# Kernel optimization log

Hardware: AMD Instinct MI355X
Metric: run time of the kernel (lower is better)

Reference implementation:

```python
import jax, jax.numpy as jnp
import numpy as np

N_NODES = 50000
N_EDGES = 1600000
IN_CH = 128
HEADS = 4
OUT_PER_HEAD = 32  # out_channels // heads with concat=True
NEG_SLOPE = 0.2    # GATConv default leaky_relu slope
SOFTMAX_EPS = 1e-16  # PyG scatter-softmax denominator eps
LN_EPS = 1e-5


def setup_inputs() -> dict:
    key = jax.random.key(0)
    ks = jax.random.split(key, 8)
    x = jax.random.normal(ks[0], (N_NODES, IN_CH), dtype=jnp.float32)
    edge_index = jax.random.randint(ks[1], (2, N_EDGES), 0, N_NODES, dtype=jnp.int32)
    W = jax.random.normal(ks[2], (IN_CH, HEADS * OUT_PER_HEAD), dtype=jnp.float32) * (1.0 / np.sqrt(IN_CH))
    att_src = jax.random.normal(ks[3], (HEADS, OUT_PER_HEAD), dtype=jnp.float32) * 0.1
    att_dst = jax.random.normal(ks[4], (HEADS, OUT_PER_HEAD), dtype=jnp.float32) * 0.1
    bias = jnp.zeros((HEADS * OUT_PER_HEAD,), dtype=jnp.float32)
    gamma = jnp.ones((HEADS * OUT_PER_HEAD,), dtype=jnp.float32)
    beta = jnp.zeros((HEADS * OUT_PER_HEAD,), dtype=jnp.float32)
    return {"x": x, "edge_index": edge_index, "W": W, "att_src": att_src,
            "att_dst": att_dst, "bias": bias, "gamma": gamma, "beta": beta}


def reference(x, edge_index, W, att_src, att_dst, bias, gamma, beta):
    N = x.shape[0]
    H, C = att_src.shape
    # GATConv default add_self_loops=True
    loop = jnp.arange(N, dtype=edge_index.dtype)
    src = jnp.concatenate([edge_index[0], loop])  # message source j
    dst = jnp.concatenate([edge_index[1], loop])  # aggregation target i

    h = (x @ W).reshape(N, H, C)                      # [N,H,C]
    a_s = jnp.einsum('nhc,hc->nh', h, att_src)        # [N,H]
    a_d = jnp.einsum('nhc,hc->nh', h, att_dst)        # [N,H]

    logits = jax.nn.leaky_relu(a_s[src] + a_d[dst], NEG_SLOPE)  # [E,H]
    # segment softmax over edges grouped by destination node
    m = jax.ops.segment_max(logits, dst, num_segments=N)        # [N,H]
    m = jnp.where(jnp.isfinite(m), m, 0.0)
    e = jnp.exp(logits - m[dst])
    s = jax.ops.segment_sum(e, dst, num_segments=N)             # [N,H]
    alpha = e / (s[dst] + SOFTMAX_EPS)                          # [E,H]

    msg = h[src] * alpha[:, :, None]                            # [E,H,C]
    out = jax.ops.segment_sum(msg, dst, num_segments=N)         # [N,H,C]
    out = out.reshape(N, H * C) + bias

    mu = out.mean(axis=-1, keepdims=True)
    var = ((out - mu) ** 2).mean(axis=-1, keepdims=True)
    y = (out - mu) / jnp.sqrt(var + LN_EPS) * gamma + beta
    return jax.nn.elu(y)
```

## Files before the change

kernel.cpp:

```cpp
#include <hip/hip_runtime.h>
#include <hip/hip_bf16.h>

typedef __hip_bfloat16 bf16;
typedef unsigned int u32;
typedef unsigned short u16;
typedef __attribute__((ext_vector_type(8))) short bf16x8;
typedef __attribute__((ext_vector_type(4))) float f32x4;

constexpr int N   = 50000;
constexpr int E   = 1600000;
constexpr int C   = 128;
constexpr int H   = 4;
constexpr int NB  = 782;
constexpr int CAP = 2560;
constexpr int NCH = 256;
constexpr int CHUNK = E / NCH;
constexpr int WT_COLS = 144;
constexpr float NEG  = 0.2f;
constexpr float SEPS = 1e-16f;
constexpr float LEPS = 1e-5f;

__device__ __forceinline__ float lo16(u32 v) { return __uint_as_float(v << 16); }
__device__ __forceinline__ float hi16(u32 v) { return __uint_as_float(v & 0xFFFF0000u); }
__device__ __forceinline__ u16 bfbits(float f) {
    __hip_bfloat16 h = __float2bfloat16(f);
    return *reinterpret_cast<u16*>(&h);
}

__global__ __launch_bounds__(256) void k0_wprep(
    const float* __restrict__ W,
    const float* __restrict__ att_s, const float* __restrict__ att_d,
    u16* __restrict__ wt_hi, u16* __restrict__ wt_lo)
{
    const int i = blockIdx.x * 256 + threadIdx.x;
    if (i >= WT_COLS * 128) return;
    const int c = i >> 7, k = i & 127;
    float w = 0.f;
    if (c < 128) {
        w = W[k * 128 + c];
    } else if (c < 136) {
        const int vc = c - 128;
        const int h = vc & 3;
        const float* att = (vc < 4) ? att_s : att_d;
        float s = 0.f;
#pragma unroll
        for (int j = 0; j < 32; ++j)
            s = fmaf(W[k * 128 + h * 32 + j], att[h * 32 + j], s);
        w = s;
    }
    const __hip_bfloat16 h = __float2bfloat16(w);
    const float fh = __bfloat162float(h);
    wt_hi[i] = *(const u16*)&h;
    wt_lo[i] = bfbits(w - fh);
}

__global__ __launch_bounds__(256, 2) void kg_gemm(
    const float* __restrict__ x,
    const u16* __restrict__ wt_hi, const u16* __restrict__ wt_lo,
    u16* __restrict__ hb, float* __restrict__ as_, float* __restrict__ ad_)
{
    const int t    = threadIdx.x;
    const int m0   = (int)blockIdx.x * 64;
    const int lane = t & 63;
    const int w    = t >> 6;
    const int bcol = lane & 15;
    const int akg  = lane >> 4;
    const int aq   = akg;

    const int arow = min(m0 + w * 16 + bcol, N - 1);
    const float* xr = x + (size_t)arow * 128;

    float4 q[8];
#pragma unroll
    for (int ks = 0; ks < 4; ++ks) {
        q[2 * ks]     = *(const float4*)(xr + ks * 32 + akg * 8);
        q[2 * ks + 1] = *(const float4*)(xr + ks * 32 + akg * 8 + 4);
    }
    __builtin_amdgcn_sched_barrier(0);

    f32x4 acc[9];
#pragma unroll
    for (int nt = 0; nt < 9; ++nt) acc[nt] = f32x4{0.f, 0.f, 0.f, 0.f};

#pragma unroll
    for (int ks = 0; ks < 4; ++ks) {
        const float4 q0 = q[2 * ks];
        const float4 q1 = q[2 * ks + 1];
        bf16x8 Ah, Al;
#define CV(idx, val) { const __hip_bfloat16 hh = __float2bfloat16(val); \
        Ah[idx] = *(const short*)&hh; \
        const __hip_bfloat16 hl = __float2bfloat16((val) - __bfloat162float(hh)); \
        Al[idx] = *(const short*)&hl; }
        CV(0, q0.x) CV(1, q0.y) CV(2, q0.z) CV(3, q0.w)
        CV(4, q1.x) CV(5, q1.y) CV(6, q1.z) CV(7, q1.w)
#undef CV
        const u16* bpk = wt_hi + bcol * 128 + ks * 32 + akg * 8;
        const u16* bqk = wt_lo + bcol * 128 + ks * 32 + akg * 8;
#pragma unroll
        for (int nt = 0; nt < 9; ++nt) {
            const bf16x8 Bh = *(const bf16x8*)(bpk + nt * 2048);
            const bf16x8 Bl = *(const bf16x8*)(bqk + nt * 2048);
            acc[nt] = __builtin_amdgcn_mfma_f32_16x16x32_bf16(Ah, Bh, acc[nt], 0, 0, 0);
            acc[nt] = __builtin_amdgcn_mfma_f32_16x16x32_bf16(Al, Bh, acc[nt], 0, 0, 0);
            acc[nt] = __builtin_amdgcn_mfma_f32_16x16x32_bf16(Ah, Bl, acc[nt], 0, 0, 0);
        }
    }

#pragma unroll
    for (int nt = 0; nt < 8; ++nt) {
        const int ch = nt * 16 + bcol;
#pragma unroll
        for (int r = 0; r < 4; ++r) {
            const int node = m0 + w * 16 + aq * 4 + r;
            if (node < N) hb[(size_t)node * 128 + ch] = bfbits(acc[nt][r]);
        }
    }

    if (bcol < 8) {
        float* dst = (bcol < 4) ? (as_ + bcol) : (ad_ + (bcol - 4));
#pragma unroll
        for (int r = 0; r < 4; ++r) {
            const int node = m0 + w * 16 + aq * 4 + r;
            if (node < N) dst[(size_t)node * H] = acc[8][r];
        }
    }
}

__global__ __launch_bounds__(256) void kc_count(
    const int* __restrict__ ei, u32* __restrict__ gcnt)
{
    __shared__ u32 lcnt[NB];
    const int t = threadIdx.x;
    const int c = blockIdx.x;
    const int base = c * CHUNK;
    for (int i = t; i < NB; i += 256) lcnt[i] = 0;
    __syncthreads();
    for (int i = t; i < CHUNK; i += 256)
        atomicAdd(&lcnt[((u32)ei[E + base + i]) >> 6], 1u);
    __syncthreads();
    for (int i = t; i < NB; i += 256) gcnt[i * NCH + c] = lcnt[i];
}

__global__ __launch_bounds__(256) void s2a_scan(
    const u32* __restrict__ gcnt, u32* __restrict__ gbase, u32* __restrict__ tot)
{
    __shared__ u32 wsum[4];
    const int b = blockIdx.x, t = threadIdx.x, lane = t & 63, w = t >> 6;
    const u32 v = gcnt[b * NCH + t];
    u32 incl = v;
#pragma unroll
    for (int off = 1; off < 64; off <<= 1) {
        u32 u = __shfl_up(incl, off, 64);
        if (lane >= off) incl += u;
    }
    if (lane == 63) wsum[w] = incl;
    __syncthreads();
    u32 wpre = 0;
#pragma unroll
    for (int i = 0; i < 4; ++i) if (i < w) wpre += wsum[i];
    gbase[b * NCH + t] = wpre + incl - v;
    if (t == 255) tot[b] = wpre + incl;
}

__global__ __launch_bounds__(64) void s2b_scan(
    const u32* __restrict__ tot, u32* __restrict__ bbase)
{
    const int t = threadIdx.x;
    u32 vals[13];
    u32 s = 0;
#pragma unroll
    for (int i = 0; i < 13; ++i) {
        int idx = t * 13 + i;
        u32 v = (idx < NB) ? tot[idx] : 0u;
        vals[i] = s; s += v;
    }
    u32 incl = s;
#pragma unroll
    for (int off = 1; off < 64; off <<= 1) {
        u32 u = __shfl_up(incl, off, 64);
        if (t >= off) incl += u;
    }
    const u32 excl = incl - s;
#pragma unroll
    for (int i = 0; i < 13; ++i) {
        int idx = t * 13 + i;
        if (idx < NB) bbase[idx] = excl + vals[i];
    }
}

__global__ __launch_bounds__(256) void kbinB(
    const int* __restrict__ ei, const u32* __restrict__ gbase,
    const u32* __restrict__ bbase, u32* __restrict__ pairs)
{
    __shared__ u32 sl[NB];
    __shared__ u32 lfill[NB];
    const int t = threadIdx.x;
    const int c = blockIdx.x;

    for (int i = t; i < NB; i += 256) {
        sl[i] = bbase[i] + gbase[(size_t)i * NCH + c];
        lfill[i] = 0u;
    }
    __syncthreads();

    const int base = c * CHUNK;
    for (int i = t; i < CHUNK; i += 256) {
        const u32 src = (u32)ei[base + i];
        const u32 dst = (u32)ei[E + base + i];
        const u32 b = dst >> 6;
        const u32 pos = atomicAdd(&lfill[b], 1u);
        pairs[sl[b] + pos] = src | ((dst & 63u) << 16);
    }
}

__global__ __launch_bounds__(256) void kfill2(
    const u32* __restrict__ pairs, const u32* __restrict__ tot,
    const u32* __restrict__ bbase, int* __restrict__ row_ptr, u16* __restrict__ col)
{
    __shared__ u32 spr[CAP];
    __shared__ u16 scol[CAP];
    __shared__ int jcnt[64], joff[64], jcur[64];
    const int b = blockIdx.x, t = threadIdx.x;
    const int base = (int)bbase[b];
    const int cntb = (int)tot[b];
    if (t < 64) jcnt[t] = 0;
    __syncthreads();

    const u32* pr = pairs + base;
    for (int i = t; i < cntb; i += 256) spr[i] = pr[i];
    __syncthreads();
    for (int i = t; i < cntb; i += 256) atomicAdd(&jcnt[spr[i] >> 16], 1);
    __syncthreads();
    if (t < 64) {
        int v = jcnt[t], incl = v;
#pragma unroll
        for (int off = 1; off < 64; off <<= 1) {
            int u = __shfl_up(incl, off, 64);
            if (t >= off) incl += u;
        }
        joff[t] = incl - v;
        const int n = b * 64 + t;
        if (n < N) row_ptr[n] = base + joff[t];
        jcur[t] = 0;
    }
    __syncthreads();
    for (int i = t; i < cntb; i += 256) {
        const u32 p = spr[i];
        const int j = p >> 16;
        const int pos = atomicAdd(&jcur[j], 1);
        scol[joff[j] + pos] = (u16)(p & 0xFFFFu);
    }
    __syncthreads();
    for (int i = t; i < cntb; i += 256) col[base + i] = scol[i];
    if (b == 0 && t == 0) row_ptr[N] = E;
}

__global__ __launch_bounds__(256) void kd_agg_ln(
    const int* __restrict__ row_ptr, const u16* __restrict__ col,
    const u32* __restrict__ hb, const float* __restrict__ as_,
    const float* __restrict__ ad_,
    const float* __restrict__ bias, const float* __restrict__ gamma,
    const float* __restrict__ beta, float* __restrict__ out, int n0)
{
    __shared__ float wlds[4][64];
    const int tid  = threadIdx.x;
    const int lane = tid & 63;
    const int wv   = __builtin_amdgcn_readfirstlane(tid >> 6);
    const int n    = __builtin_amdgcn_readfirstlane(n0 + (int)blockIdx.x * 4 + (tid >> 6));
    if (n >= N) return;

    const int head  = lane >> 4;
    const int eoff  = lane & 15;
    const int wbase = head << 4;
    float* __restrict__ wrow = wlds[wv];

    const float adn = ad_[n * H + head];
    const float asn = as_[n * H + head];

    float ls = asn + adn;
    ls = fmaxf(ls, NEG * ls);
    const float wself = __expf(ls);
    float den = (eoff == 0) ? wself : 0.f;
    const u32 hvs = hb[n * 64 + lane];
    float num0 = wself * lo16(hvs);
    float num1 = wself * hi16(hvs);

    const int k0  = row_ptr[n];
    const int deg = row_ptr[n + 1] - k0;
    const int ntiles = (deg + 15) >> 4;

    const int cnt0 = deg < 16 ? deg : 16;
    const int cnt1 = (deg - 16) < 16 ? (deg - 16) : 16;
    int colv_cur = (eoff < cnt0) ? (int)col[k0 + eoff]      : 0;
    int colv_nxt = (eoff < cnt1) ? (int)col[k0 + 16 + eoff] : 0;
    float a_cur  = as_[colv_cur * H + head];
    int cntc = cnt0, cntn = cnt1;

    int k = k0;
    for (int t = 0; t < ntiles; ++t, k += 16) {
        const int rem2 = deg - 16 * (t + 2);
        const int cnt2 = rem2 < 16 ? rem2 : 16;
        const int cf_raw = (int)col[k + 32 + eoff];
        const int colv_f = (eoff < cnt2) ? cf_raw : 0;

        float le = a_cur + adn;
        le = fmaxf(le, NEG * le);
        const float w = (eoff < cntc) ? __expf(le) : 0.f;
        den += w;
        wrow[lane] = w;
        const int colc = colv_cur;

#define GL(i) const u32* rp##i = hb + ((size_t)(u32)__builtin_amdgcn_readlane(colc, i) << 6); \
              const u32 v##i = rp##i[lane];
        GL(0) GL(1) GL(2) GL(3) GL(4) GL(5) GL(6) GL(7)
        GL(8) GL(9) GL(10) GL(11) GL(12) GL(13) GL(14) GL(15)
#undef GL
        __builtin_amdgcn_sched_barrier(0);

        const float a_n = as_[colv_nxt * H + head];
        __builtin_amdgcn_sched_barrier(0);

        {
            const float4 wa = *(const float4*)(wrow + wbase + 0);
            num0 = fmaf(wa.x, lo16(v0), num0);  num1 = fmaf(wa.x, hi16(v0), num1);
            num0 = fmaf(wa.y, lo16(v1), num0);  num1 = fmaf(wa.y, hi16(v1), num1);
            num0 = fmaf(wa.z, lo16(v2), num0);  num1 = fmaf(wa.z, hi16(v2), num1);
            num0 = fmaf(wa.w, lo16(v3), num0);  num1 = fmaf(wa.w, hi16(v3), num1);
            const float4 wb = *(const float4*)(wrow + wbase + 4);
            num0 = fmaf(wb.x, lo16(v4), num0);  num1 = fmaf(wb.x, hi16(v4), num1);
            num0 = fmaf(wb.y, lo16(v5), num0);  num1 = fmaf(wb.y, hi16(v5), num1);
            num0 = fmaf(wb.z, lo16(v6), num0);  num1 = fmaf(wb.z, hi16(v6), num1);
            num0 = fmaf(wb.w, lo16(v7), num0);  num1 = fmaf(wb.w, hi16(v7), num1);
            const float4 wc = *(const float4*)(wrow + wbase + 8);
            num0 = fmaf(wc.x, lo16(v8), num0);  num1 = fmaf(wc.x, hi16(v8), num1);
            num0 = fmaf(wc.y, lo16(v9), num0);  num1 = fmaf(wc.y, hi16(v9), num1);
            num0 = fmaf(wc.z, lo16(v10), num0); num1 = fmaf(wc.z, hi16(v10), num1);
            num0 = fmaf(wc.w, lo16(v11), num0); num1 = fmaf(wc.w, hi16(v11), num1);
            const float4 wd = *(const float4*)(wrow + wbase + 12);
            num0 = fmaf(wd.x, lo16(v12), num0); num1 = fmaf(wd.x, hi16(v12), num1);
            num0 = fmaf(wd.y, lo16(v13), num0); num1 = fmaf(wd.y, hi16(v13), num1);
            num0 = fmaf(wd.z, lo16(v14), num0); num1 = fmaf(wd.z, hi16(v14), num1);
            num0 = fmaf(wd.w, lo16(v15), num0); num1 = fmaf(wd.w, hi16(v15), num1);
        }

        colv_cur = colv_nxt; colv_nxt = colv_f;
        a_cur = a_n;
        cntc = cntn; cntn = cnt2;
    }

#pragma unroll
    for (int off = 1; off < 16; off <<= 1) den += __shfl_xor(den, off, 64);

    const int c0 = lane * 2;
    const float inv_den = 1.f / (den + SEPS);
    const float2 bi = *(const float2*)(bias + c0);
    float v0 = num0 * inv_den + bi.x;
    float v1 = num1 * inv_den + bi.y;

    float sum = v0 + v1;
#pragma unroll
    for (int off = 32; off; off >>= 1) sum += __shfl_xor(sum, off, 64);
    const float mu = sum * (1.0f / C);
    const float d0 = v0 - mu, d1 = v1 - mu;
    float sq = d0 * d0 + d1 * d1;
#pragma unroll
    for (int off = 32; off; off >>= 1) sq += __shfl_xor(sq, off, 64);
    const float inv = rsqrtf(sq * (1.0f / C) + LEPS);
    const float2 ga = *(const float2*)(gamma + c0);
    const float2 be = *(const float2*)(beta  + c0);
    float y0 = d0 * inv * ga.x + be.x;
    float y1 = d1 * inv * ga.y + be.y;
    y0 = y0 > 0.f ? y0 : __expf(y0) - 1.f;
    y1 = y1 > 0.f ? y1 : __expf(y1) - 1.f;
    float2 o; o.x = y0; o.y = y1;
    *(float2*)(out + (size_t)n * C + c0) = o;
}

extern "C" void kernel_launch(void* const* d_in, const int* in_sizes, int n_in,
                              void* d_out, int out_size, void* d_ws, size_t ws_size,
                              hipStream_t stream)
{
    const float* x     = (const float*)d_in[0];
    const int*   ei    = (const int*)  d_in[1];
    const float* W     = (const float*)d_in[2];
    const float* att_s = (const float*)d_in[3];
    const float* att_d = (const float*)d_in[4];
    const float* bias  = (const float*)d_in[5];
    const float* gamma = (const float*)d_in[6];
    const float* beta  = (const float*)d_in[7];
    float* out = (float*)d_out;

    char* p = (char*)d_ws;
    bf16*  hb      = (bf16*)p;   p += (size_t)N * C * sizeof(bf16);
    float* as_     = (float*)p;  p += (size_t)N * H * sizeof(float);
    float* ad_     = (float*)p;  p += (size_t)N * H * sizeof(float);
    u32*   pairs   = (u32*)p;    p += (size_t)E * sizeof(u32);
    u16*   col     = (u16*)p;    p += ((size_t)(E + 64) * sizeof(u16) + 15) & ~(size_t)15;
    int*   row_ptr = (int*)p;    p += ((size_t)(N + 1) * sizeof(int) + 15) & ~(size_t)15;
    u32*   gcnt    = (u32*)p;    p += (size_t)NB * NCH * sizeof(u32);
    u32*   gbase   = (u32*)p;    p += (size_t)NB * NCH * sizeof(u32);
    u32*   tot     = (u32*)p;    p += (((size_t)NB * sizeof(u32)) + 15) & ~(size_t)15;
    u32*   bbase   = (u32*)p;    p += (((size_t)NB * sizeof(u32)) + 15) & ~(size_t)15;
    u16*   wt_hi   = (u16*)p;    p += (size_t)WT_COLS * 128 * sizeof(u16);
    u16*   wt_lo   = (u16*)p;

    k0_wprep<<<(WT_COLS * 128 + 255) / 256, 256, 0, stream>>>(W, att_s, att_d, wt_hi, wt_lo);
    kg_gemm<<<NB, 256, 0, stream>>>(x, wt_hi, wt_lo, (u16*)hb, as_, ad_);
    kc_count<<<NCH, 256, 0, stream>>>(ei, gcnt);
    s2a_scan<<<NB, 256, 0, stream>>>(gcnt, gbase, tot);
    s2b_scan<<<1, 64, 0, stream>>>(tot, bbase);
    kbinB<<<NCH, 256, 0, stream>>>(ei, gbase, bbase, pairs);
    kfill2<<<NB, 256, 0, stream>>>(pairs, tot, bbase, row_ptr, col);
    kd_agg_ln<<<(25000 * 64) / 256, 256, 0, stream>>>(
        row_ptr, col, (const u32*)hb, as_, ad_, bias, gamma, beta, out, 0);
    kd_agg_ln<<<(25000 * 64) / 256, 256, 0, stream>>>(
        row_ptr, col, (const u32*)hb, as_, ad_, bias, gamma, beta, out, 25000);
}
```

Before: 227.8 us.

## Process two row tiles per wave in GEMM and double-buffer B fragments

The projection GEMM now handles 128 rows per block, with each wave computing two 16-row groups. This lets every B-fragment load from the split-bf16 weight tables be reused twice. B fragments for successive k-steps are prefetched into alternating register buffers, with schedule barriers to overlap loads with MFMA work. The cost is higher register pressure from 18 accumulators plus four B buffers, which may lower occupancy or cause spills. The grid also shrinks to about half as many blocks, which gives less parallelism for only 50k rows.

```diff
diff --git a/kernel.cpp b/kernel.cpp
--- a/kernel.cpp
+++ b/kernel.cpp
@@ -60,68 +60,108 @@
     u16* __restrict__ hb, float* __restrict__ as_, float* __restrict__ ad_)
 {
     const int t    = threadIdx.x;
-    const int m0   = (int)blockIdx.x * 64;
+    const int m0   = (int)blockIdx.x * 128;
     const int lane = t & 63;
     const int w    = t >> 6;
     const int bcol = lane & 15;
     const int akg  = lane >> 4;
-    const int aq   = akg;
-
-    const int arow = min(m0 + w * 16 + bcol, N - 1);
-    const float* xr = x + (size_t)arow * 128;
-
-    float4 q[8];
+
+    const int r0 = min(m0 + w * 32 + bcol,      N - 1);
+    const int r1 = min(m0 + w * 32 + 16 + bcol, N - 1);
+    const float* x0 = x + (size_t)r0 * 128 + akg * 8;
+    const float* x1 = x + (size_t)r1 * 128 + akg * 8;
+
+    float4 q[16];
 #pragma unroll
     for (int ks = 0; ks < 4; ++ks) {
-        q[2 * ks]     = *(const float4*)(xr + ks * 32 + akg * 8);
-        q[2 * ks + 1] = *(const float4*)(xr + ks * 32 + akg * 8 + 4);
+        q[4 * ks + 0] = *(const float4*)(x0 + ks * 32);
+        q[4 * ks + 1] = *(const float4*)(x0 + ks * 32 + 4);
+        q[4 * ks + 2] = *(const float4*)(x1 + ks * 32);
+        q[4 * ks + 3] = *(const float4*)(x1 + ks * 32 + 4);
     }
     __builtin_amdgcn_sched_barrier(0);
 
-    f32x4 acc[9];
-#pragma unroll
-    for (int nt = 0; nt < 9; ++nt) acc[nt] = f32x4{0.f, 0.f, 0.f, 0.f};
-
+    const u16* bp = wt_hi + bcol * 128 + akg * 8;
+    const u16* bq = wt_lo + bcol * 128 + akg * 8;
+    bf16x8 BhA[9], BlA[9], BhB[9], BlB[9];
+
+#define LOADB(BH, BL, ks)                                           \
+    _Pragma("unroll")                                               \
+    for (int nt = 0; nt < 9; ++nt) {                                \
+        BH[nt] = *(const bf16x8*)(bp + nt * 2048 + (ks) * 32);      \
+        BL[nt] = *(const bf16x8*)(bq + nt * 2048 + (ks) * 32);      \
+    }
+
+    LOADB(BhA, BlA, 0)
+    __builtin_amdgcn_sched_barrier(0);
+
+    bf16x8 Ah[2][4], Al[2][4];
 #pragma unroll
     for (int ks = 0; ks < 4; ++ks) {
-        const float4 q0 = q[2 * ks];
-        const float4 q1 = q[2 * ks + 1];
-        bf16x8 Ah, Al;
-#define CV(idx, val) { const __hip_bfloat16 hh = __float2bfloat16(val); \
-        Ah[idx] = *(const short*)&hh; \
-        const __hip_bfloat16 hl = __float2bfloat16((val) - __bfloat162float(hh)); \
-        Al[idx] = *(const short*)&hl; }
-        CV(0, q0.x) CV(1, q0.y) CV(2, q0.z) CV(3, q0.w)
-        CV(4, q1.x) CV(5, q1.y) CV(6, q1.z) CV(7, q1.w)
-#undef CV
-        const u16* bpk = wt_hi + bcol * 128 + ks * 32 + akg * 8;
-        const u16* bqk = wt_lo + bcol * 128 + ks * 32 + akg * 8;
-#pragma unroll
-        for (int nt = 0; nt < 9; ++nt) {
-            const bf16x8 Bh = *(const bf16x8*)(bpk + nt * 2048);
-            const bf16x8 Bl = *(const bf16x8*)(bqk + nt * 2048);
-            acc[nt] = __builtin_amdgcn_mfma_f32_16x16x32_bf16(Ah, Bh, acc[nt], 0, 0, 0);
-            acc[nt] = __builtin_amdgcn_mfma_f32_16x16x32_bf16(Al, Bh, acc[nt], 0, 0, 0);
-            acc[nt] = __builtin_amdgcn_mfma_f32_16x16x32_bf16(Ah, Bl, acc[nt], 0, 0, 0);
+#pragma unroll
+        for (int rg = 0; rg < 2; ++rg) {
+            const float4 qa = q[4 * ks + 2 * rg];
+            const float4 qb = q[4 * ks + 2 * rg + 1];
+            const float f[8] = {qa.x, qa.y, qa.z, qa.w, qb.x, qb.y, qb.z, qb.w};
+#pragma unroll
+            for (int j = 0; j < 8; ++j) {
+                const __hip_bfloat16 hh = __float2bfloat16(f[j]);
+                Ah[rg][ks][j] = *(const short*)&hh;
+                const __hip_bfloat16 hl = __float2bfloat16(f[j] - __bfloat162float(hh));
+                Al[rg][ks][j] = *(const short*)&hl;
+            }
         }
     }
 
-#pragma unroll
-    for (int nt = 0; nt < 8; ++nt) {
-        const int ch = nt * 16 + bcol;
-#pragma unroll
-        for (int r = 0; r < 4; ++r) {
-            const int node = m0 + w * 16 + aq * 4 + r;
-            if (node < N) hb[(size_t)node * 128 + ch] = bfbits(acc[nt][r]);
+    f32x4 acc[2][9];
+#pragma unroll
+    for (int rg = 0; rg < 2; ++rg)
+#pragma unroll
+        for (int nt = 0; nt < 9; ++nt) acc[rg][nt] = f32x4{0.f, 0.f, 0.f, 0.f};
+
+#define STEP(BHc, BLc, ks)                                          \
+    _Pragma("unroll")                                               \
+    for (int rg = 0; rg < 2; ++rg) {                                \
+        _Pragma("unroll")                                           \
+        for (int nt = 0; nt < 9; ++nt) {                            \
+            acc[rg][nt] = __builtin_amdgcn_mfma_f32_16x16x32_bf16(Ah[rg][ks], BHc[nt], acc[rg][nt], 0, 0, 0); \
+            acc[rg][nt] = __builtin_amdgcn_mfma_f32_16x16x32_bf16(Al[rg][ks], BHc[nt], acc[rg][nt], 0, 0, 0); \
+            acc[rg][nt] = __builtin_amdgcn_mfma_f32_16x16x32_bf16(Ah[rg][ks], BLc[nt], acc[rg][nt], 0, 0, 0); \
+        }                                                           \
+    }
+
+    LOADB(BhB, BlB, 1)
+    __builtin_amdgcn_sched_barrier(0);
+    STEP(BhA, BlA, 0)
+    LOADB(BhA, BlA, 2)
+    __builtin_amdgcn_sched_barrier(0);
+    STEP(BhB, BlB, 1)
+    LOADB(BhB, BlB, 3)
+    __builtin_amdgcn_sched_barrier(0);
+    STEP(BhA, BlA, 2)
+    STEP(BhB, BlB, 3)
+
+#undef STEP
+#undef LOADB
+
+#pragma unroll
+    for (int rg = 0; rg < 2; ++rg) {
+#pragma unroll
+        for (int nt = 0; nt < 8; ++nt) {
+            const int ch = nt * 16 + bcol;
+#pragma unroll
+            for (int r = 0; r < 4; ++r) {
+                const int node = m0 + w * 32 + rg * 16 + akg * 4 + r;
+                if (node < N) hb[(size_t)node * 128 + ch] = bfbits(acc[rg][nt][r]);
+            }
         }
-    }
-
-    if (bcol < 8) {
-        float* dst = (bcol < 4) ? (as_ + bcol) : (ad_ + (bcol - 4));
-#pragma unroll
-        for (int r = 0; r < 4; ++r) {
-            const int node = m0 + w * 16 + aq * 4 + r;
-            if (node < N) dst[(size_t)node * H] = acc[8][r];
+        if (bcol < 8) {
+            float* dst = (bcol < 4) ? (as_ + bcol) : (ad_ + (bcol - 4));
+#pragma unroll
+            for (int r = 0; r < 4; ++r) {
+                const int node = m0 + w * 32 + rg * 16 + akg * 4 + r;
+                if (node < N) dst[(size_t)node * H] = acc[rg][8][r];
+            }
         }
     }
 }
@@ -405,7 +445,7 @@
     u16*   wt_lo   = (u16*)p;
 
     k0_wprep<<<(WT_COLS * 128 + 255) / 256, 256, 0, stream>>>(W, att_s, att_d, wt_hi, wt_lo);
-    kg_gemm<<<NB, 256, 0, stream>>>(x, wt_hi, wt_lo, (u16*)hb, as_, ad_);
+    kg_gemm<<<(N + 127) / 128, 256, 0, stream>>>(x, wt_hi, wt_lo, (u16*)hb, as_, ad_);
     kc_count<<<NCH, 256, 0, stream>>>(ei, gcnt);
     s2a_scan<<<NB, 256, 0, stream>>>(gcnt, gbase, tot);
     s2b_scan<<<1, 64, 0, stream>>>(tot, bbase);
```

Result: slower. 239.3 us (+5.0%).
